# Kernel tuning notes

Measured on AMD Instinct MI355X. Metric: run time of the kernel, lower is better.

Reference implementation:

```python
import jax, jax.numpy as jnp
import numpy as np

EMBED_DIM = 1024
NUM_HEADS = 16
HEAD_DIM = EMBED_DIM // NUM_HEADS
ROPE_BASE = 10000.0


def _rope_angles(seq_len, head_dim):
    inv_freq = 1.0 / (ROPE_BASE ** (jnp.arange(0, head_dim, 2, dtype=jnp.float32) / head_dim))  # [D/2]
    pos = jnp.arange(seq_len, dtype=jnp.float32)
    ang = pos[:, None] * inv_freq[None, :]  # [S, D/2]
    return jnp.cos(ang), jnp.sin(ang)


def _apply_rope(t, cos, sin):
    # t: [B, H, S, D]; rotate-half convention
    d2 = t.shape[-1] // 2
    t1, t2 = t[..., :d2], t[..., d2:]
    return jnp.concatenate([t1 * cos - t2 * sin, t2 * cos + t1 * sin], axis=-1)


def setup_inputs() -> dict:
    key = jax.random.key(0)
    ks = jax.random.split(key, 6)
    B, S, E = 1, 4096, EMBED_DIM
    x = jax.random.normal(ks[0], (B, S, E), dtype=jnp.float32)
    # causal mask: True means masked-out (upper triangle above diagonal)
    mask = jnp.triu(jnp.ones((S, S), dtype=bool), k=1)[None, None, :, :]
    scale = 0.02
    wqkv_w = jax.random.normal(ks[1], (E, 3 * E), dtype=jnp.float32) * scale
    wqkv_b = jax.random.normal(ks[2], (3 * E,), dtype=jnp.float32) * scale
    out_w = jax.random.normal(ks[3], (E, E), dtype=jnp.float32) * scale
    out_b = jax.random.normal(ks[4], (E,), dtype=jnp.float32) * scale
    return {"x": x, "mask": mask, "wqkv_w": wqkv_w, "wqkv_b": wqkv_b, "out_w": out_w, "out_b": out_b}


def reference(x, mask, wqkv_w, wqkv_b, out_w, out_b):
    B, S, E = x.shape
    H, D = NUM_HEADS, HEAD_DIM
    qkv = x @ wqkv_w + wqkv_b  # [B, S, 3E]
    q, k, v = jnp.split(qkv, 3, axis=-1)
    # [B, S, E] -> [B, H, S, D]
    q = q.reshape(B, S, H, D).transpose(0, 2, 1, 3)
    k = k.reshape(B, S, H, D).transpose(0, 2, 1, 3)
    v = v.reshape(B, S, H, D).transpose(0, 2, 1, 3)
    cos, sin = _rope_angles(S, D)  # [S, D/2]
    q = _apply_rope(q, cos, sin)
    k = _apply_rope(k, cos, sin)
    scores = jnp.einsum('bhqd,bhkd->bhqk', q, k) * (D ** -0.5)  # [B, H, S, S]
    scores = jnp.where(mask[:, :, -S:, :], -jnp.inf, scores)
    weights = jax.nn.softmax(scores, axis=-1)
    ctx = jnp.einsum('bhqk,bhkd->bhqd', weights, v)  # [B, H, S, D]
    ctx = ctx.transpose(0, 2, 1, 3).reshape(B, S, E)
    return ctx @ out_w + out_b
```

## Files before the change

kernel.cpp:

```cpp
#include <hip/hip_runtime.h>
#include <hip/hip_bf16.h>
#include <math.h>

#define S_LEN 4096
#define EMB   1024
#define E3    3072
#define NH    16
#define HD    64

typedef unsigned short u16;
typedef short          bfrag __attribute__((ext_vector_type(8)));
typedef float          ffrag __attribute__((ext_vector_type(4)));
typedef unsigned short us8   __attribute__((ext_vector_type(8)));
typedef unsigned short us4   __attribute__((ext_vector_type(4)));

__device__ __forceinline__ u16 f2bf(float f) {
    union { float f; unsigned u; } v; v.f = f;
    unsigned r = v.u + 0x7fffu + ((v.u >> 16) & 1u);
    return (u16)(r >> 16);
}
__device__ __forceinline__ float bf2f(u16 b) {
    union { unsigned u; float f; } v; v.u = ((unsigned)b) << 16;
    return v.f;
}
__device__ __forceinline__ unsigned pack_bf16_trunc(float lo, float hi) {
    union { float f; unsigned u; } a, b; a.f = lo; b.f = hi;
    return __builtin_amdgcn_perm(b.u, a.u, 0x07060302u);
}
__device__ __forceinline__ void gld16(const void* g, void* l) {
    __builtin_amdgcn_global_load_lds(
        (const __attribute__((address_space(1))) unsigned int*)g,
        (__attribute__((address_space(3))) unsigned int*)l, 16, 0, 0);
}

__global__ __launch_bounds__(256)
void cast_bf16_kernel(const float* __restrict__ in, u16* __restrict__ out) {
    const size_t i = ((size_t)blockIdx.x * 256 + threadIdx.x) * 8;
    float4 a = *(const float4*)(in + i);
    float4 b = *(const float4*)(in + i + 4);
    us8 o;
    o[0]=f2bf(a.x); o[1]=f2bf(a.y); o[2]=f2bf(a.z); o[3]=f2bf(a.w);
    o[4]=f2bf(b.x); o[5]=f2bf(b.y); o[6]=f2bf(b.z); o[7]=f2bf(b.w);
    *(us8*)(out + i) = o;
}

__global__ __launch_bounds__(256)
void transpose_cast_kernel(const float* __restrict__ in, u16* __restrict__ out,
                           int R, int C) {
    __shared__ u16 T[64][72];
    const int r0 = blockIdx.x * 64, c0 = blockIdx.y * 64;
    const int t = threadIdx.x;
    const int rr = t >> 2, cc = (t & 3) * 16;

    const float* ip = in + (size_t)(r0 + rr) * C + c0 + cc;
    u16 tmp[16];
    #pragma unroll
    for (int i4 = 0; i4 < 4; i4++) {
        float4 v = ((const float4*)ip)[i4];
        tmp[4*i4+0]=f2bf(v.x); tmp[4*i4+1]=f2bf(v.y);
        tmp[4*i4+2]=f2bf(v.z); tmp[4*i4+3]=f2bf(v.w);
    }
    #pragma unroll
    for (int i8 = 0; i8 < 2; i8++) {
        us8 vv;
        #pragma unroll
        for (int j = 0; j < 8; j++) vv[j] = tmp[8*i8+j];
        *(us8*)&T[rr][cc + 8*i8] = vv;
    }
    __syncthreads();

    const int oc = t >> 2, orr = (t & 3) * 16;
    u16 ot[16];
    #pragma unroll
    for (int j = 0; j < 16; j++) ot[j] = T[orr + j][oc];
    u16* op = out + (size_t)(c0 + oc) * R + r0 + orr;
    #pragma unroll
    for (int i8 = 0; i8 < 2; i8++) {
        us8 vv;
        #pragma unroll
        for (int j = 0; j < 8; j++) vv[j] = ot[8*i8+j];
        *(us8*)(op + 8*i8) = vv;
    }
}

__global__ __launch_bounds__(256)
void transpose_v_kernel(const u16* __restrict__ qkvb, u16* __restrict__ vt) {
    __shared__ u16 T[64][72];
    const int s0 = blockIdx.x * 64, h = blockIdx.y;
    const int t = threadIdx.x;
    const int rr = t >> 2, cc = (t & 3) * 16;

    const u16* ip = qkvb + (size_t)(s0 + rr) * E3 + 2 * EMB + h * HD + cc;
    *(us8*)&T[rr][cc]     = *(const us8*)ip;
    *(us8*)&T[rr][cc + 8] = *(const us8*)(ip + 8);
    __syncthreads();

    const int od = t >> 2, os = (t & 3) * 16;
    u16 ot[16];
    #pragma unroll
    for (int j = 0; j < 16; j++) ot[j] = T[os + j][od];
    u16* op = vt + ((size_t)h * HD + od) * S_LEN + s0 + os;
    #pragma unroll
    for (int i8 = 0; i8 < 2; i8++) {
        us8 vv;
        #pragma unroll
        for (int j = 0; j < 8; j++) vv[j] = ot[8*i8+j];
        *(us8*)(op + 8*i8) = vv;
    }
}

__global__ __launch_bounds__(256)
void rope_bf16_kernel(u16* __restrict__ qkvb) {
    const int idx = blockIdx.x * blockDim.x + threadIdx.x;
    const int i = idx & 31;
    const int h = (idx >> 5) & (NH - 1);
    const int s = idx >> 9;

    const float inv_freq = exp2f(-(float)i * (13.287712379549449f / 32.0f));
    float sn, cs;
    sincosf((float)s * inv_freq, &sn, &cs);
    const float SC = 0.125f * 1.44269504088896f;

    size_t base = (size_t)s * E3 + h * HD;
    {
        float t1 = bf2f(qkvb[base + i]), t2 = bf2f(qkvb[base + i + 32]);
        qkvb[base + i]      = f2bf((t1 * cs - t2 * sn) * SC);
        qkvb[base + i + 32] = f2bf((t2 * cs + t1 * sn) * SC);
    }
    base += EMB;
    {
        float t1 = bf2f(qkvb[base + i]), t2 = bf2f(qkvb[base + i + 32]);
        qkvb[base + i]      = f2bf(t1 * cs - t2 * sn);
        qkvb[base + i + 32] = f2bf(t2 * cs + t1 * sn);
    }
}

template <int OUT_BF16>
__global__ __launch_bounds__(256, 2)
void gemm_bt_kernel(const u16* __restrict__ A, const u16* __restrict__ Bt,
                    const float* __restrict__ bias, void* __restrict__ Cv,
                    int M, int N, int K) {
    __shared__ u16 As[2][128][32];
    __shared__ u16 Bs[2][128][32];

    const int tid = threadIdx.x;
    const int w = tid >> 6, L = tid & 63;
    const int col = L & 15, quad = L >> 4;
    const int wm = w & 1, wn = w >> 1;
    const int m0 = blockIdx.x * 128, n0 = blockIdx.y * 128;

    ffrag acc[4][4];
    #pragma unroll
    for (int a = 0; a < 4; a++)
        #pragma unroll
        for (int b = 0; b < 4; b++)
            #pragma unroll
            for (int r = 0; r < 4; r++) acc[a][b][r] = 0.f;

    const int srow = L >> 2;
    const int schk = L & 3;

    #pragma unroll
    for (int t = 0; t < 2; t++) {
        const int rg = (2 * w + t) * 16;
        gld16(A  + (size_t)(m0 + rg + srow) * K + schk * 8, &As[0][rg][0]);
        gld16(Bt + (size_t)(n0 + rg + srow) * K + schk * 8, &Bs[0][rg][0]);
    }
    __syncthreads();

    int buf = 0;
    for (int k0 = 0; k0 < K; k0 += 32, buf ^= 1) {
        if (k0 + 32 < K) {
            #pragma unroll
            for (int t = 0; t < 2; t++) {
                const int rg = (2 * w + t) * 16;
                gld16(A  + (size_t)(m0 + rg + srow) * K + k0 + 32 + schk * 8,
                      &As[buf ^ 1][rg][0]);
                gld16(Bt + (size_t)(n0 + rg + srow) * K + k0 + 32 + schk * 8,
                      &Bs[buf ^ 1][rg][0]);
            }
        }

        bfrag af[4], bf[4];
        #pragma unroll
        for (int mt = 0; mt < 4; mt++)
            af[mt] = *(const bfrag*)&As[buf][64 * wm + 16 * mt + col][8 * quad];
        #pragma unroll
        for (int nt = 0; nt < 4; nt++)
            bf[nt] = *(const bfrag*)&Bs[buf][64 * wn + 16 * nt + col][8 * quad];
        #pragma unroll
        for (int mt = 0; mt < 4; mt++)
            #pragma unroll
            for (int nt = 0; nt < 4; nt++)
                acc[mt][nt] = __builtin_amdgcn_mfma_f32_16x16x32_bf16(
                    af[mt], bf[nt], acc[mt][nt], 0, 0, 0);

        __syncthreads();
    }

    float bv[4];
    #pragma unroll
    for (int nt = 0; nt < 4; nt++) bv[nt] = bias[n0 + 64 * wn + 16 * nt + col];

    #pragma unroll
    for (int mt = 0; mt < 4; mt++) {
        #pragma unroll
        for (int r = 0; r < 4; r++) {
            const int m = m0 + 64 * wm + 16 * mt + 4 * quad + r;
            #pragma unroll
            for (int nt = 0; nt < 4; nt++) {
                const int n = n0 + 64 * wn + 16 * nt + col;
                const float val = acc[mt][nt][r] + bv[nt];
                if (OUT_BF16) ((u16*)Cv)[(size_t)m * N + n] = f2bf(val);
                else          ((float*)Cv)[(size_t)m * N + n] = val;
            }
        }
    }
}

__global__ __launch_bounds__(256, 4)
void flash5_kernel(const u16* __restrict__ qkvb, const u16* __restrict__ vt,
                   u16* __restrict__ ctxb) {
    __shared__ u16 QP[4][16][64];
    __shared__ u16 Ks[2][64][64];
    __shared__ u16 Vs[2][64][64];

    const int id = blockIdx.x;
    const int j  = (id >> 3) & 63;
    const int h  = (id & 7) | ((id >> 9) << 3);
    const int qi = (j < 32) ? j : 95 - j;
    const int q0 = qi * 64;
    const int ntk = qi + 1;

    const int tid = threadIdx.x;
    const int w = tid >> 6, L = tid & 63;
    const int col = L & 15, quad = L >> 4;
    const int lr = L >> 3, lp = L & 7;
    const int lc = lp ^ lr;

    const size_t kArow = (size_t)(16 * w + lr) * E3 + EMB + h * HD + lc * 8;
    const size_t vArow = ((size_t)h * HD + 16 * w + lr) * S_LEN + lc * 8;

    #pragma unroll
    for (int u = 0; u < 2; u++) {
        gld16(qkvb + (size_t)(q0 + 16 * w + 8 * u + lr) * E3 + h * HD + lc * 8,
              &QP[w][8 * u][0]);
        gld16(qkvb + kArow + (size_t)(8 * u) * E3, &Ks[0][16 * w + 8 * u][0]);
        gld16(vt + vArow + (size_t)(8 * u) * S_LEN, &Vs[0][16 * w + 8 * u][0]);
    }
    __syncthreads();

    bfrag qf[2];
    #pragma unroll
    for (int ks = 0; ks < 2; ks++)
        qf[ks] = *(const bfrag*)
            ((const char*)&QP[w][col][0] + 16 * ((4 * ks + quad) ^ (col & 7)));

    bfrag ones;
    #pragma unroll
    for (int i = 0; i < 8; i++) ones[i] = (short)0x3F80;

    ffrag o[4], ol;
    #pragma unroll
    for (int d4 = 0; d4 < 4; d4++)
        #pragma unroll
        for (int r = 0; r < 4; r++) o[d4][r] = 0.f;
    #pragma unroll
    for (int r = 0; r < 4; r++) ol[r] = 0.f;

    #pragma unroll 1
    for (int t = 0; t < ntk; t++) {
        const int buf = t & 1;
        if (t + 1 < ntk) {
            const size_t ko = kArow + (size_t)(t + 1) * 64 * E3;
            const size_t vo = vArow + (size_t)(t + 1) * 64;
            #pragma unroll
            for (int u = 0; u < 2; u++) {
                gld16(qkvb + ko + (size_t)(8 * u) * E3, &Ks[buf ^ 1][16 * w + 8 * u][0]);
                gld16(vt + vo + (size_t)(8 * u) * S_LEN, &Vs[buf ^ 1][16 * w + 8 * u][0]);
            }
        }

        ffrag st[4];
        #pragma unroll
        for (int t4 = 0; t4 < 4; t4++)
            #pragma unroll
            for (int r = 0; r < 4; r++) st[t4][r] = 0.f;
        #pragma unroll
        for (int ks = 0; ks < 2; ks++) {
            bfrag kf[4];
            #pragma unroll
            for (int t4 = 0; t4 < 4; t4++)
                kf[t4] = *(const bfrag*)
                    &Ks[buf][16 * t4 + col][(((4 * ks + quad) ^ (col & 7)) * 8)];
            #pragma unroll
            for (int t4 = 0; t4 < 4; t4++)
                st[t4] = __builtin_amdgcn_mfma_f32_16x16x32_bf16(
                    kf[t4], qf[ks], st[t4], 0, 0, 0);
        }

        if (t == ntk - 1) {
            const int qloc = 16 * w + col;
            #pragma unroll
            for (int t4 = 0; t4 < 4; t4++) {
                const int key0 = 16 * t4 + 4 * quad;
                #pragma unroll
                for (int r = 0; r < 4; r++)
                    if (key0 + r > qloc) st[t4][r] = -3.0e38f;
            }
        }

        #pragma unroll
        for (int t4 = 0; t4 < 4; t4++) {
            float pr[4];
            #pragma unroll
            for (int r = 0; r < 4; r++) pr[r] = exp2f(st[t4][r]);
            uint2 pk;
            pk.x = pack_bf16_trunc(pr[0], pr[1]);
            pk.y = pack_bf16_trunc(pr[2], pr[3]);
            const int c2 = (2 * t4 + (quad >> 1)) ^ (col & 7);
            *(uint2*)((char*)&QP[w][col][0] + 16 * c2 + 8 * (quad & 1)) = pk;
        }

        #pragma unroll
        for (int ks = 0; ks < 2; ks++) {
            bfrag vf[4];
            #pragma unroll
            for (int d4 = 0; d4 < 4; d4++)
                vf[d4] = *(const bfrag*)
                    &Vs[buf][16 * d4 + col][(((4 * ks + quad) ^ (col & 7)) * 8)];
            bfrag pf = *(const bfrag*)
                ((const char*)&QP[w][col][0] + 16 * ((4 * ks + quad) ^ (col & 7)));
            #pragma unroll
            for (int d4 = 0; d4 < 4; d4++)
                o[d4] = __builtin_amdgcn_mfma_f32_16x16x32_bf16(
                    vf[d4], pf, o[d4], 0, 0, 0);
            ol = __builtin_amdgcn_mfma_f32_16x16x32_bf16(ones, pf, ol, 0, 0, 0);
        }

        __syncthreads();
    }

    const float inv = 1.0f / ol[0];
    const int qg = q0 + 16 * w + col;
    #pragma unroll
    for (int d4 = 0; d4 < 4; d4++) {
        us4 pk;
        #pragma unroll
        for (int r = 0; r < 4; r++) pk[r] = f2bf(o[d4][r] * inv);
        *(us4*)&ctxb[(size_t)qg * EMB + h * HD + 16 * d4 + 4 * quad] = pk;
    }
}

extern "C" void kernel_launch(void* const* d_in, const int* in_sizes, int n_in,
                              void* d_out, int out_size, void* d_ws, size_t ws_size,
                              hipStream_t stream) {
    const float* x      = (const float*)d_in[0];
    const float* wqkv_w = (const float*)d_in[2];
    const float* wqkv_b = (const float*)d_in[3];
    const float* out_w  = (const float*)d_in[4];
    const float* out_b  = (const float*)d_in[5];
    float* out = (float*)d_out;

    u16* qkvb = (u16*)d_ws;
    u16* ctxb = qkvb + (size_t)S_LEN * E3;
    u16* xb   = ctxb + (size_t)S_LEN * EMB;
    u16* wt   = xb   + (size_t)S_LEN * EMB;
    u16* owt  = wt   + (size_t)E3 * EMB;
    u16* vtb  = owt  + (size_t)EMB * EMB;

    dim3 blk(256);

    cast_bf16_kernel<<<dim3(S_LEN * EMB / (256 * 8)), blk, 0, stream>>>(x, xb);
    transpose_cast_kernel<<<dim3(EMB / 64, E3 / 64), blk, 0, stream>>>(
        wqkv_w, wt, EMB, E3);
    transpose_cast_kernel<<<dim3(EMB / 64, EMB / 64), blk, 0, stream>>>(
        out_w, owt, EMB, EMB);

    gemm_bt_kernel<1><<<dim3(S_LEN / 128, E3 / 128), blk, 0, stream>>>(
        xb, wt, wqkv_b, qkvb, S_LEN, E3, EMB);

    rope_bf16_kernel<<<dim3(S_LEN * NH * 32 / 256), blk, 0, stream>>>(qkvb);
    transpose_v_kernel<<<dim3(S_LEN / 64, NH), blk, 0, stream>>>(qkvb, vtb);

    flash5_kernel<<<dim3(1024), blk, 0, stream>>>(qkvb, vtb, ctxb);

    gemm_bt_kernel<0><<<dim3(S_LEN / 128, EMB / 128), blk, 0, stream>>>(
        ctxb, owt, out_b, out, S_LEN, EMB, EMB);
}
```

Measured before the change: 267.4 us.

## Fuse RoPE into QKV GEMM epilogue, widen flash tiles, narrow output GEMM

```diff
diff --git a/kernel.cpp b/kernel.cpp
--- a/kernel.cpp
+++ b/kernel.cpp
@@ -18,10 +18,6 @@
     union { float f; unsigned u; } v; v.f = f;
     unsigned r = v.u + 0x7fffu + ((v.u >> 16) & 1u);
     return (u16)(r >> 16);
-}
-__device__ __forceinline__ float bf2f(u16 b) {
-    union { unsigned u; float f; } v; v.u = ((unsigned)b) << 16;
-    return v.f;
 }
 __device__ __forceinline__ unsigned pack_bf16_trunc(float lo, float hi) {
     union { float f; unsigned u; } a, b; a.f = lo; b.f = hi;
@@ -109,51 +105,27 @@
     }
 }
 
-__global__ __launch_bounds__(256)
-void rope_bf16_kernel(u16* __restrict__ qkvb) {
-    const int idx = blockIdx.x * blockDim.x + threadIdx.x;
-    const int i = idx & 31;
-    const int h = (idx >> 5) & (NH - 1);
-    const int s = idx >> 9;
-
-    const float inv_freq = exp2f(-(float)i * (13.287712379549449f / 32.0f));
-    float sn, cs;
-    sincosf((float)s * inv_freq, &sn, &cs);
-    const float SC = 0.125f * 1.44269504088896f;
-
-    size_t base = (size_t)s * E3 + h * HD;
-    {
-        float t1 = bf2f(qkvb[base + i]), t2 = bf2f(qkvb[base + i + 32]);
-        qkvb[base + i]      = f2bf((t1 * cs - t2 * sn) * SC);
-        qkvb[base + i + 32] = f2bf((t2 * cs + t1 * sn) * SC);
-    }
-    base += EMB;
-    {
-        float t1 = bf2f(qkvb[base + i]), t2 = bf2f(qkvb[base + i + 32]);
-        qkvb[base + i]      = f2bf(t1 * cs - t2 * sn);
-        qkvb[base + i + 32] = f2bf(t2 * cs + t1 * sn);
-    }
-}
-
-template <int OUT_BF16>
-__global__ __launch_bounds__(256, 2)
+template <int OUT_BF16, int NT, int ROPE, int MINW>
+__global__ __launch_bounds__(256, MINW)
 void gemm_bt_kernel(const u16* __restrict__ A, const u16* __restrict__ Bt,
                     const float* __restrict__ bias, void* __restrict__ Cv,
                     int M, int N, int K) {
+    constexpr int BN = 32 * NT;
+    constexpr int WS = 16 * NT;
     __shared__ u16 As[2][128][32];
-    __shared__ u16 Bs[2][128][32];
+    __shared__ u16 Bs[2][BN][32];
 
     const int tid = threadIdx.x;
     const int w = tid >> 6, L = tid & 63;
     const int col = L & 15, quad = L >> 4;
     const int wm = w & 1, wn = w >> 1;
-    const int m0 = blockIdx.x * 128, n0 = blockIdx.y * 128;
-
-    ffrag acc[4][4];
+    const int m0 = blockIdx.x * 128, n0 = blockIdx.y * BN;
+
+    ffrag acc[4][NT];
     #pragma unroll
     for (int a = 0; a < 4; a++)
         #pragma unroll
-        for (int b = 0; b < 4; b++)
+        for (int b = 0; b < NT; b++)
             #pragma unroll
             for (int r = 0; r < 4; r++) acc[a][b][r] = 0.f;
 
@@ -163,7 +135,11 @@
     #pragma unroll
     for (int t = 0; t < 2; t++) {
         const int rg = (2 * w + t) * 16;
-        gld16(A  + (size_t)(m0 + rg + srow) * K + schk * 8, &As[0][rg][0]);
+        gld16(A + (size_t)(m0 + rg + srow) * K + schk * 8, &As[0][rg][0]);
+    }
+    #pragma unroll
+    for (int t = 0; t < NT / 2; t++) {
+        const int rg = (w * (NT / 2) + t) * 16;
         gld16(Bt + (size_t)(n0 + rg + srow) * K + schk * 8, &Bs[0][rg][0]);
     }
     __syncthreads();
@@ -174,63 +150,95 @@
             #pragma unroll
             for (int t = 0; t < 2; t++) {
                 const int rg = (2 * w + t) * 16;
-                gld16(A  + (size_t)(m0 + rg + srow) * K + k0 + 32 + schk * 8,
+                gld16(A + (size_t)(m0 + rg + srow) * K + k0 + 32 + schk * 8,
                       &As[buf ^ 1][rg][0]);
+            }
+            #pragma unroll
+            for (int t = 0; t < NT / 2; t++) {
+                const int rg = (w * (NT / 2) + t) * 16;
                 gld16(Bt + (size_t)(n0 + rg + srow) * K + k0 + 32 + schk * 8,
                       &Bs[buf ^ 1][rg][0]);
             }
         }
 
-        bfrag af[4], bf[4];
+        bfrag af[4], bf[NT];
         #pragma unroll
         for (int mt = 0; mt < 4; mt++)
             af[mt] = *(const bfrag*)&As[buf][64 * wm + 16 * mt + col][8 * quad];
         #pragma unroll
-        for (int nt = 0; nt < 4; nt++)
-            bf[nt] = *(const bfrag*)&Bs[buf][64 * wn + 16 * nt + col][8 * quad];
+        for (int nt = 0; nt < NT; nt++)
+            bf[nt] = *(const bfrag*)&Bs[buf][WS * wn + 16 * nt + col][8 * quad];
         #pragma unroll
         for (int mt = 0; mt < 4; mt++)
             #pragma unroll
-            for (int nt = 0; nt < 4; nt++)
+            for (int nt = 0; nt < NT; nt++)
                 acc[mt][nt] = __builtin_amdgcn_mfma_f32_16x16x32_bf16(
                     af[mt], bf[nt], acc[mt][nt], 0, 0, 0);
 
         __syncthreads();
     }
 
-    float bv[4];
-    #pragma unroll
-    for (int nt = 0; nt < 4; nt++) bv[nt] = bias[n0 + 64 * wn + 16 * nt + col];
-
-    #pragma unroll
-    for (int mt = 0; mt < 4; mt++) {
-        #pragma unroll
-        for (int r = 0; r < 4; r++) {
-            const int m = m0 + 64 * wm + 16 * mt + 4 * quad + r;
-            #pragma unroll
-            for (int nt = 0; nt < 4; nt++) {
-                const int n = n0 + 64 * wn + 16 * nt + col;
-                const float val = acc[mt][nt][r] + bv[nt];
-                if (OUT_BF16) ((u16*)Cv)[(size_t)m * N + n] = f2bf(val);
-                else          ((float*)Cv)[(size_t)m * N + n] = val;
-            }
-        }
-    }
-}
-
-__global__ __launch_bounds__(256, 4)
-void flash5_kernel(const u16* __restrict__ qkvb, const u16* __restrict__ vt,
+    float bv[NT];
+    #pragma unroll
+    for (int nt = 0; nt < NT; nt++) bv[nt] = bias[n0 + WS * wn + 16 * nt + col];
+
+    if (ROPE && n0 < 2 * EMB) {
+        const float SCq = (n0 < EMB) ? 0.125f * 1.44269504088896f : 1.0f;
+        const float C = 13.287712379549449f / 32.0f;
+        float invf[2];
+        invf[0] = exp2f(-(float)col * C);
+        invf[1] = exp2f(-(float)(col + 16) * C);
+        #pragma unroll
+        for (int mt = 0; mt < 4; mt++) {
+            #pragma unroll
+            for (int r = 0; r < 4; r++) {
+                const int mrow = m0 + 64 * wm + 16 * mt + 4 * quad + r;
+                const float fs = (float)mrow;
+                u16* cp = (u16*)Cv + (size_t)mrow * N + n0 + 64 * wn + col;
+                #pragma unroll
+                for (int pr = 0; pr < 2; pr++) {
+                    float sn, cs;
+                    sincosf(fs * invf[pr], &sn, &cs);
+                    const float t1 = acc[mt][pr][r] + bv[pr];
+                    const float t2 = acc[mt][pr + 2][r] + bv[pr + 2];
+                    cp[16 * pr]      = f2bf((t1 * cs - t2 * sn) * SCq);
+                    cp[16 * pr + 32] = f2bf((t2 * cs + t1 * sn) * SCq);
+                }
+            }
+        }
+    } else {
+        #pragma unroll
+        for (int mt = 0; mt < 4; mt++) {
+            #pragma unroll
+            for (int r = 0; r < 4; r++) {
+                const int m = m0 + 64 * wm + 16 * mt + 4 * quad + r;
+                #pragma unroll
+                for (int nt = 0; nt < NT; nt++) {
+                    const int n = n0 + WS * wn + 16 * nt + col;
+                    const float val = acc[mt][nt][r] + bv[nt];
+                    if (OUT_BF16) ((u16*)Cv)[(size_t)m * N + n] = f2bf(val);
+                    else          ((float*)Cv)[(size_t)m * N + n] = val;
+                }
+            }
+        }
+    }
+}
+
+__global__ __launch_bounds__(256, 2)
+void flash6_kernel(const u16* __restrict__ qkvb, const u16* __restrict__ vt,
                    u16* __restrict__ ctxb) {
-    __shared__ u16 QP[4][16][64];
+    __shared__ u16 QP[4][32][64];
     __shared__ u16 Ks[2][64][64];
     __shared__ u16 Vs[2][64][64];
 
     const int id = blockIdx.x;
-    const int j  = (id >> 3) & 63;
-    const int h  = (id & 7) | ((id >> 9) << 3);
-    const int qi = (j < 32) ? j : 95 - j;
-    const int q0 = qi * 64;
-    const int ntk = qi + 1;
+    const int j  = (id >> 3) & 31;
+    const int hi = id >> 8;
+    const int h  = (id & 7) | (hi << 3);
+    const int zig = (j < 16) ? j : 47 - j;
+    const int qi  = hi ? (31 - zig) : zig;
+    const int q0  = qi * 128;
+    const int ntk = 2 * qi + 2;
 
     const int tid = threadIdx.x;
     const int w = tid >> 6, L = tid & 63;
@@ -238,35 +246,46 @@
     const int lr = L >> 3, lp = L & 7;
     const int lc = lp ^ lr;
 
+    const int nwt = ntk - (w < 2 ? 1 : 0);
+
     const size_t kArow = (size_t)(16 * w + lr) * E3 + EMB + h * HD + lc * 8;
     const size_t vArow = ((size_t)h * HD + 16 * w + lr) * S_LEN + lc * 8;
 
     #pragma unroll
+    for (int u = 0; u < 4; u++)
+        gld16(qkvb + (size_t)(q0 + 32 * w + 8 * u + lr) * E3 + h * HD + lc * 8,
+              &QP[w][8 * u][0]);
+    #pragma unroll
     for (int u = 0; u < 2; u++) {
-        gld16(qkvb + (size_t)(q0 + 16 * w + 8 * u + lr) * E3 + h * HD + lc * 8,
-              &QP[w][8 * u][0]);
         gld16(qkvb + kArow + (size_t)(8 * u) * E3, &Ks[0][16 * w + 8 * u][0]);
         gld16(vt + vArow + (size_t)(8 * u) * S_LEN, &Vs[0][16 * w + 8 * u][0]);
     }
     __syncthreads();
 
-    bfrag qf[2];
-    #pragma unroll
-    for (int ks = 0; ks < 2; ks++)
-        qf[ks] = *(const bfrag*)
-            ((const char*)&QP[w][col][0] + 16 * ((4 * ks + quad) ^ (col & 7)));
+    bfrag qf[2][2];
+    #pragma unroll
+    for (int i = 0; i < 2; i++)
+        #pragma unroll
+        for (int ks = 0; ks < 2; ks++)
+            qf[i][ks] = *(const bfrag*)
+                ((const char*)&QP[w][16 * i + col][0] +
+                 16 * ((4 * ks + quad) ^ (col & 7)));
 
     bfrag ones;
     #pragma unroll
     for (int i = 0; i < 8; i++) ones[i] = (short)0x3F80;
 
-    ffrag o[4], ol;
+    ffrag o[4][2], ol[2];
     #pragma unroll
     for (int d4 = 0; d4 < 4; d4++)
         #pragma unroll
-        for (int r = 0; r < 4; r++) o[d4][r] = 0.f;
-    #pragma unroll
-    for (int r = 0; r < 4; r++) ol[r] = 0.f;
+        for (int i = 0; i < 2; i++)
+            #pragma unroll
+            for (int r = 0; r < 4; r++) o[d4][i][r] = 0.f;
+    #pragma unroll
+    for (int i = 0; i < 2; i++)
+        #pragma unroll
+        for (int r = 0; r < 4; r++) ol[i][r] = 0.f;
 
     #pragma unroll 1
     for (int t = 0; t < ntk; t++) {
@@ -276,79 +295,106 @@
             const size_t vo = vArow + (size_t)(t + 1) * 64;
             #pragma unroll
             for (int u = 0; u < 2; u++) {
-                gld16(qkvb + ko + (size_t)(8 * u) * E3, &Ks[buf ^ 1][16 * w + 8 * u][0]);
-                gld16(vt + vo + (size_t)(8 * u) * S_LEN, &Vs[buf ^ 1][16 * w + 8 * u][0]);
-            }
-        }
-
-        ffrag st[4];
-        #pragma unroll
-        for (int t4 = 0; t4 < 4; t4++)
-            #pragma unroll
-            for (int r = 0; r < 4; r++) st[t4][r] = 0.f;
-        #pragma unroll
-        for (int ks = 0; ks < 2; ks++) {
-            bfrag kf[4];
+                gld16(qkvb + ko + (size_t)(8 * u) * E3,
+                      &Ks[buf ^ 1][16 * w + 8 * u][0]);
+                gld16(vt + vo + (size_t)(8 * u) * S_LEN,
+                      &Vs[buf ^ 1][16 * w + 8 * u][0]);
+            }
+        }
+
+        if (t < nwt) {
+            ffrag st[4][2];
             #pragma unroll
             for (int t4 = 0; t4 < 4; t4++)
-                kf[t4] = *(const bfrag*)
-                    &Ks[buf][16 * t4 + col][(((4 * ks + quad) ^ (col & 7)) * 8)];
-            #pragma unroll
-            for (int t4 = 0; t4 < 4; t4++)
-                st[t4] = __builtin_amdgcn_mfma_f32_16x16x32_bf16(
-                    kf[t4], qf[ks], st[t4], 0, 0, 0);
-        }
-
-        if (t == ntk - 1) {
-            const int qloc = 16 * w + col;
-            #pragma unroll
-            for (int t4 = 0; t4 < 4; t4++) {
-                const int key0 = 16 * t4 + 4 * quad;
-                #pragma unroll
-                for (int r = 0; r < 4; r++)
-                    if (key0 + r > qloc) st[t4][r] = -3.0e38f;
-            }
-        }
-
-        #pragma unroll
-        for (int t4 = 0; t4 < 4; t4++) {
-            float pr[4];
-            #pragma unroll
-            for (int r = 0; r < 4; r++) pr[r] = exp2f(st[t4][r]);
-            uint2 pk;
-            pk.x = pack_bf16_trunc(pr[0], pr[1]);
-            pk.y = pack_bf16_trunc(pr[2], pr[3]);
-            const int c2 = (2 * t4 + (quad >> 1)) ^ (col & 7);
-            *(uint2*)((char*)&QP[w][col][0] + 16 * c2 + 8 * (quad & 1)) = pk;
-        }
-
-        #pragma unroll
-        for (int ks = 0; ks < 2; ks++) {
-            bfrag vf[4];
-            #pragma unroll
-            for (int d4 = 0; d4 < 4; d4++)
-                vf[d4] = *(const bfrag*)
-                    &Vs[buf][16 * d4 + col][(((4 * ks + quad) ^ (col & 7)) * 8)];
-            bfrag pf = *(const bfrag*)
-                ((const char*)&QP[w][col][0] + 16 * ((4 * ks + quad) ^ (col & 7)));
-            #pragma unroll
-            for (int d4 = 0; d4 < 4; d4++)
-                o[d4] = __builtin_amdgcn_mfma_f32_16x16x32_bf16(
-                    vf[d4], pf, o[d4], 0, 0, 0);
-            ol = __builtin_amdgcn_mfma_f32_16x16x32_bf16(ones, pf, ol, 0, 0, 0);
+                #pragma unroll
+                for (int i = 0; i < 2; i++)
+                    #pragma unroll
+                    for (int r = 0; r < 4; r++) st[t4][i][r] = 0.f;
+            #pragma unroll
+            for (int ks = 0; ks < 2; ks++) {
+                bfrag kf[4];
+                #pragma unroll
+                for (int t4 = 0; t4 < 4; t4++)
+                    kf[t4] = *(const bfrag*)
+                        &Ks[buf][16 * t4 + col][(((4 * ks + quad) ^ (col & 7)) * 8)];
+                #pragma unroll
+                for (int t4 = 0; t4 < 4; t4++)
+                    #pragma unroll
+                    for (int i = 0; i < 2; i++)
+                        st[t4][i] = __builtin_amdgcn_mfma_f32_16x16x32_bf16(
+                            kf[t4], qf[i][ks], st[t4][i], 0, 0, 0);
+            }
+
+            if (t == nwt - 1) {
+                #pragma unroll
+                for (int i = 0; i < 2; i++) {
+                    const int qrel = 32 * (w & 1) + 16 * i + col;
+                    #pragma unroll
+                    for (int t4 = 0; t4 < 4; t4++) {
+                        const int key0 = 16 * t4 + 4 * quad;
+                        #pragma unroll
+                        for (int r = 0; r < 4; r++)
+                            if (key0 + r > qrel) st[t4][i][r] = -3.0e38f;
+                    }
+                }
+            }
+
+            #pragma unroll
+            for (int i = 0; i < 2; i++) {
+                const int prow = 16 * i + col;
+                #pragma unroll
+                for (int t4 = 0; t4 < 4; t4++) {
+                    float pr[4];
+                    #pragma unroll
+                    for (int r = 0; r < 4; r++) pr[r] = exp2f(st[t4][i][r]);
+                    uint2 pk;
+                    pk.x = pack_bf16_trunc(pr[0], pr[1]);
+                    pk.y = pack_bf16_trunc(pr[2], pr[3]);
+                    const int c2 = (2 * t4 + (quad >> 1)) ^ (col & 7);
+                    *(uint2*)((char*)&QP[w][prow][0] + 16 * c2 + 8 * (quad & 1)) = pk;
+                }
+            }
+
+            #pragma unroll
+            for (int ks = 0; ks < 2; ks++) {
+                bfrag vf[4];
+                #pragma unroll
+                for (int d4 = 0; d4 < 4; d4++)
+                    vf[d4] = *(const bfrag*)
+                        &Vs[buf][16 * d4 + col][(((4 * ks + quad) ^ (col & 7)) * 8)];
+                bfrag pf[2];
+                #pragma unroll
+                for (int i = 0; i < 2; i++)
+                    pf[i] = *(const bfrag*)
+                        ((const char*)&QP[w][16 * i + col][0] +
+                         16 * ((4 * ks + quad) ^ (col & 7)));
+                #pragma unroll
+                for (int d4 = 0; d4 < 4; d4++)
+                    #pragma unroll
+                    for (int i = 0; i < 2; i++)
+                        o[d4][i] = __builtin_amdgcn_mfma_f32_16x16x32_bf16(
+                            vf[d4], pf[i], o[d4][i], 0, 0, 0);
+                #pragma unroll
+                for (int i = 0; i < 2; i++)
+                    ol[i] = __builtin_amdgcn_mfma_f32_16x16x32_bf16(
+                        ones, pf[i], ol[i], 0, 0, 0);
+            }
         }
 
         __syncthreads();
     }
 
-    const float inv = 1.0f / ol[0];
-    const int qg = q0 + 16 * w + col;
-    #pragma unroll
-    for (int d4 = 0; d4 < 4; d4++) {
-        us4 pk;
-        #pragma unroll
-        for (int r = 0; r < 4; r++) pk[r] = f2bf(o[d4][r] * inv);
-        *(us4*)&ctxb[(size_t)qg * EMB + h * HD + 16 * d4 + 4 * quad] = pk;
+    #pragma unroll
+    for (int i = 0; i < 2; i++) {
+        const float inv = 1.0f / ol[i][0];
+        const int qg = q0 + 32 * w + 16 * i + col;
+        #pragma unroll
+        for (int d4 = 0; d4 < 4; d4++) {
+            us4 pk;
+            #pragma unroll
+            for (int r = 0; r < 4; r++) pk[r] = f2bf(o[d4][i][r] * inv);
+            *(us4*)&ctxb[(size_t)qg * EMB + h * HD + 16 * d4 + 4 * quad] = pk;
+        }
     }
 }
 
@@ -377,14 +423,13 @@
     transpose_cast_kernel<<<dim3(EMB / 64, EMB / 64), blk, 0, stream>>>(
         out_w, owt, EMB, EMB);
 
-    gemm_bt_kernel<1><<<dim3(S_LEN / 128, E3 / 128), blk, 0, stream>>>(
+    gemm_bt_kernel<1, 4, 1, 3><<<dim3(S_LEN / 128, E3 / 128), blk, 0, stream>>>(
         xb, wt, wqkv_b, qkvb, S_LEN, E3, EMB);
 
-    rope_bf16_kernel<<<dim3(S_LEN * NH * 32 / 256), blk, 0, stream>>>(qkvb);
     transpose_v_kernel<<<dim3(S_LEN / 64, NH), blk, 0, stream>>>(qkvb, vtb);
 
-    flash5_kernel<<<dim3(1024), blk, 0, stream>>>(qkvb, vtb, ctxb);
-
-    gemm_bt_kernel<0><<<dim3(S_LEN / 128, EMB / 128), blk, 0, stream>>>(
+    flash6_kernel<<<dim3(512), blk, 0, stream>>>(qkvb, vtb, ctxb);
+
+    gemm_bt_kernel<0, 2, 0, 2><<<dim3(S_LEN / 128, EMB / 64), blk, 0, stream>>>(
         ctxb, owt, out_b, out, S_LEN, EMB, EMB);
 }
```

New measurement: 257.5 us. -3.7%, faster.
